# Optimization experiments

Measured on AMD Instinct MI355X. Metric: run time of the kernel, lower is better.

## Reference

```python
import jax, jax.numpy as jnp
import numpy as np

IN_FEATS, N_HIDDEN, NUM_LAYERS, N_CLASSES, CLS_HIDDEN = 166, 76, 2, 2, 510
T, N, E = 3, 100000, 1600000
RRELU_SLOPE = (1.0 / 8.0 + 1.0 / 3.0) / 2.0  # eval-mode RReLU = leaky relu with mean slope


def setup_inputs() -> dict:
    key = jax.random.key(0)
    ks = jax.random.split(key, 24)
    d = {}
    d['feats'] = jax.random.normal(ks[0], (T, N, IN_FEATS), jnp.float32)
    d['src'] = jax.random.randint(ks[1], (T, E), 0, N, jnp.int32)
    d['dst'] = jax.random.randint(ks[2], (T, E), 0, N, jnp.int32)
    # TopK scorers (uniform +-1/sqrt(feats))
    s0 = 1.0 / np.sqrt(IN_FEATS)
    s1 = 1.0 / np.sqrt(N_HIDDEN)
    d['scorer0'] = jax.random.uniform(ks[3], (IN_FEATS, 1), jnp.float32, -s0, s0)
    d['scorer1'] = jax.random.uniform(ks[4], (N_HIDDEN, 1), jnp.float32, -s1, s1)
    # GCN weights (xavier-ish)
    d['gcn_w0'] = jax.random.normal(ks[5], (IN_FEATS, N_HIDDEN), jnp.float32) * np.sqrt(2.0 / (IN_FEATS + N_HIDDEN))
    d['gcn_w1'] = jax.random.normal(ks[6], (N_HIDDEN, N_HIDDEN), jnp.float32) * np.sqrt(2.0 / (2 * N_HIDDEN))
    # GRU params, torch layout: W_ih [3H, H_in], W_hh [3H, H], gate order (r, z, n)
    g = 1.0 / np.sqrt(N_HIDDEN)
    H3 = 3 * N_HIDDEN
    d['gru0_wih'] = jax.random.uniform(ks[7], (H3, N_HIDDEN), jnp.float32, -g, g)
    d['gru0_whh'] = jax.random.uniform(ks[8], (H3, N_HIDDEN), jnp.float32, -g, g)
    d['gru0_bih'] = jax.random.uniform(ks[9], (H3,), jnp.float32, -g, g)
    d['gru0_bhh'] = jax.random.uniform(ks[10], (H3,), jnp.float32, -g, g)
    d['gru1_wih'] = jax.random.uniform(ks[11], (H3, N_HIDDEN), jnp.float32, -g, g)
    d['gru1_whh'] = jax.random.uniform(ks[12], (H3, N_HIDDEN), jnp.float32, -g, g)
    d['gru1_bih'] = jax.random.uniform(ks[13], (H3,), jnp.float32, -g, g)
    d['gru1_bhh'] = jax.random.uniform(ks[14], (H3,), jnp.float32, -g, g)
    # MLP
    m1 = 1.0 / np.sqrt(N_HIDDEN)
    m2 = 1.0 / np.sqrt(CLS_HIDDEN)
    d['mlp_w1'] = jax.random.uniform(ks[15], (N_HIDDEN, CLS_HIDDEN), jnp.float32, -m1, m1)
    d['mlp_b1'] = jax.random.uniform(ks[16], (CLS_HIDDEN,), jnp.float32, -m1, m1)
    d['mlp_w2'] = jax.random.uniform(ks[17], (CLS_HIDDEN, N_CLASSES), jnp.float32, -m2, m2)
    d['mlp_b2'] = jax.random.uniform(ks[18], (N_CLASSES,), jnp.float32, -m2, m2)
    return d


def _topk_pool(x, scorer, k):
    # x: [N, F]; returns X_tilde: [F, k]
    scores = (x @ scorer).ravel() / jnp.linalg.norm(scorer)
    vals, idx = jax.lax.top_k(scores, k)
    out = x[idx] * jnp.tanh(vals)[:, None]  # [k, F]
    return out.T


def _gru_step(x, h, wih, whh, bih, bhh):
    # x: [B, H_in], h: [B, H]; torch GRU gate order r, z, n
    gx = x @ wih.T + bih
    gh = h @ whh.T + bhh
    H = h.shape[1]
    rx, zx, nx = gx[:, :H], gx[:, H:2 * H], gx[:, 2 * H:]
    rh, zh, nh = gh[:, :H], gh[:, H:2 * H], gh[:, 2 * H:]
    r = jax.nn.sigmoid(rx + rh)
    z = jax.nn.sigmoid(zx + zh)
    n = jnp.tanh(nx + r * nh)
    return (1.0 - z) * n + z * h


def _graph_conv(x, W, src, dst, n_nodes):
    # DGL GraphConv, norm='both', bias=False, RReLU (eval) activation
    deg_out = jnp.zeros((n_nodes,), x.dtype).at[src].add(1.0)
    deg_in = jnp.zeros((n_nodes,), x.dtype).at[dst].add(1.0)
    norm_src = jnp.clip(deg_out, 1.0, None) ** -0.5
    norm_dst = jnp.clip(deg_in, 1.0, None) ** -0.5
    h = (x * norm_src[:, None]) @ W  # project first (small out dim)
    agg = jax.ops.segment_sum(h[src], dst, num_segments=n_nodes)
    out = agg * norm_dst[:, None]
    return jnp.where(out >= 0, out, out * RRELU_SLOPE)


def reference(feats, src, dst, scorer0, scorer1, gcn_w0, gcn_w1,
              gru0_wih, gru0_whh, gru0_bih, gru0_bhh,
              gru1_wih, gru1_whh, gru1_bih, gru1_bhh,
              mlp_w1, mlp_b1, mlp_w2, mlp_b2):
    scorers = [scorer0, scorer1]
    gcn_ws = [gcn_w0, gcn_w1]
    grus = [(gru0_wih, gru0_whh, gru0_bih, gru0_bhh),
            (gru1_wih, gru1_whh, gru1_bih, gru1_bhh)]
    feat_list = [feats[t] for t in range(T)]
    for i in range(NUM_LAYERS):
        W = gcn_ws[i]
        wih, whh, bih, bhh = grus[i]
        for t in range(T):
            x_tilde = _topk_pool(feat_list[t], scorers[i], N_HIDDEN)  # [F, k]
            W = _gru_step(x_tilde, W, wih, whh, bih, bhh)  # evolve weights
            feat_list[t] = _graph_conv(feat_list[t], W, src[t], dst[t], N)
    h = feat_list[-1]
    h = jax.nn.relu(h @ mlp_w1 + mlp_b1)
    return h @ mlp_w2 + mlp_b2
```

## Files before the change

### kernel.cpp

```cpp
#include <hip/hip_runtime.h>
#include <math.h>

#define NN 100000
#define EE 1600000
#define F0 166
#define HID 76
#define H3 228
#define CHID 510
#define SLOPE 0.22916666666666666f
#define CAND_MAX 4096
#define NBIN 4096
#define HPAD 20

#define BSH 9
#define BSZ 512
#define NBKT 196
#define CH 4096
#define NCHK 391
#define NBAND 13
#define AGG_NWG 7422

__device__ __forceinline__ unsigned f2key(float f){
    unsigned u = __float_as_uint(f);
    return (u & 0x80000000u) ? ~u : (u | 0x80000000u);
}
__device__ __forceinline__ float key2f(unsigned k){
    unsigned u = (k & 0x80000000u) ? (k & 0x7fffffffu) : ~k;
    return __uint_as_float(u);
}

__global__ void scorer_norms_k(const float* __restrict__ s0, const float* __restrict__ s1,
                               float* __restrict__ outn){
    __shared__ float red[256];
    int tid = threadIdx.x;
    float a = 0.f;
    for (int k = tid; k < F0; k += 256) a += s0[k]*s0[k];
    red[tid] = a; __syncthreads();
    for (int s = 128; s > 0; s >>= 1){ if (tid < s) red[tid] += red[tid+s]; __syncthreads(); }
    if (tid == 0) outn[0] = 1.0f/sqrtf(red[0]);
    __syncthreads();
    float b = 0.f;
    for (int k = tid; k < HID; k += 256) b += s1[k]*s1[k];
    red[tid] = b; __syncthreads();
    for (int s = 128; s > 0; s >>= 1){ if (tid < s) red[tid] += red[tid+s]; __syncthreads(); }
    if (tid == 0) outn[1] = 1.0f/sqrtf(red[0]);
}

__global__ void pad_k(const float* __restrict__ w1, const float* __restrict__ b1,
                      const float* __restrict__ w2, float* __restrict__ w1t,
                      float* __restrict__ b1p, float* __restrict__ w2p){
    int idx = blockIdx.x*256 + threadIdx.x;
    if (idx < 512*HID){
        int j = idx / HID, k = idx - j*HID;
        w1t[idx] = (j < CHID) ? w1[k*CHID + j] : 0.f;
    }
    if (idx < 512)  b1p[idx] = (idx < CHID)   ? b1[idx] : 0.f;
    if (idx < 1024) w2p[idx] = (idx < CHID*2) ? w2[idx] : 0.f;
}


__global__ __launch_bounds__(256) void p1_hist_k(const int* __restrict__ src, const int* __restrict__ dst,
                                                 int* __restrict__ bhS, int* __restrict__ bhD){
    __shared__ int hS[NBKT], hD[NBKT];
    int t = blockIdx.y, blk = blockIdx.x, tid = threadIdx.x;
    for (int i = tid; i < NBKT; i += 256){ hS[i] = 0; hD[i] = 0; }
    __syncthreads();
    size_t ebase = (size_t)t*EE + (size_t)blk*CH;
    int m = EE - blk*CH; if (m > CH) m = CH;
    for (int j = tid; j < m; j += 256){
        atomicAdd(&hS[src[ebase + j] >> BSH], 1);
        atomicAdd(&hD[dst[ebase + j] >> BSH], 1);
    }
    __syncthreads();
    for (int i = tid; i < NBKT; i += 256){
        bhS[((size_t)t*NBKT + i)*NCHK + blk] = hS[i];
        bhD[((size_t)t*NBKT + i)*NCHK + blk] = hD[i];
    }
}

__global__ __launch_bounds__(512) void p2_scan_k(int* __restrict__ bhS, int* __restrict__ bhD,
                                                 int* __restrict__ ctS, int* __restrict__ ctD){
    __shared__ int sd[512];
    int b = blockIdx.x, t = blockIdx.y, tid = threadIdx.x;
    for (int a = 0; a < 2; a++){
        int* bh = a ? bhD : bhS;
        int* ct = a ? ctD : ctS;
        int* row = bh + ((size_t)t*NBKT + b)*NCHK;
        int v = (tid < NCHK) ? row[tid] : 0;
        sd[tid] = v; __syncthreads();
        for (int off = 1; off < 512; off <<= 1){
            int x = (tid >= off) ? sd[tid - off] : 0;
            __syncthreads();
            sd[tid] += x;
            __syncthreads();
        }
        if (tid < NCHK) row[tid] = sd[tid] - v;
        if (tid == 511) ct[t*NBKT + b] = sd[511];
        __syncthreads();
    }
}

__global__ __launch_bounds__(256) void p3_base_k(const int* __restrict__ ctS, const int* __restrict__ ctD,
                                                 int* __restrict__ bbS, int* __restrict__ bbD){
    __shared__ int sd[256];
    int tid = threadIdx.x;
    for (int a = 0; a < 2; a++){
        const int* ct = a ? ctD : ctS;
        int* bb = a ? bbD : bbS;
        for (int t = 0; t < 3; t++){
            int v = (tid < NBKT) ? ct[t*NBKT + tid] : 0;
            sd[tid] = v; __syncthreads();
            for (int off = 1; off < 256; off <<= 1){
                int x = (tid >= off) ? sd[tid - off] : 0;
                __syncthreads();
                sd[tid] += x;
                __syncthreads();
            }
            if (tid < NBKT) bb[t*(NBKT+1) + tid] = sd[tid] - v;
            if (tid == 0)   bb[t*(NBKT+1) + NBKT] = EE;
            __syncthreads();
        }
    }
}

__global__ __launch_bounds__(256) void p4_scatter_k(const int* __restrict__ src, const int* __restrict__ dst,
                                                    const int* __restrict__ bhS, const int* __restrict__ bhD,
                                                    const int* __restrict__ bbS, const int* __restrict__ bbD,
                                                    int* __restrict__ srcpart,
                                                    unsigned long long* __restrict__ pairpart){
    __shared__ int baseS[NBKT], baseD[NBKT], cS[NBKT], cD[NBKT];
    int t = blockIdx.y, blk = blockIdx.x, tid = threadIdx.x;
    for (int i = tid; i < NBKT; i += 256){
        baseS[i] = bbS[t*(NBKT+1) + i] + bhS[((size_t)t*NBKT + i)*NCHK + blk];
        baseD[i] = bbD[t*(NBKT+1) + i] + bhD[((size_t)t*NBKT + i)*NCHK + blk];
        cS[i] = 0; cD[i] = 0;
    }
    __syncthreads();
    size_t ebase = (size_t)t*EE + (size_t)blk*CH;
    int m = EE - blk*CH; if (m > CH) m = CH;
    int* sp = srcpart + (size_t)t*EE;
    unsigned long long* pp = pairpart + (size_t)t*EE;
    for (int j = tid; j < m; j += 256){
        int s = src[ebase + j], d = dst[ebase + j];
        int bs = s >> BSH, bd = d >> BSH;
        int r0 = atomicAdd(&cS[bs], 1);
        sp[baseS[bs] + r0] = s;
        int r1 = atomicAdd(&cD[bd], 1);
        pp[baseD[bd] + r1] = ((unsigned long long)(unsigned)s << 32) | (unsigned)d;
    }
}

__global__ __launch_bounds__(256) void p5_degO_k(const int* __restrict__ srcpart,
                                                 const int* __restrict__ bbS,
                                                 float* __restrict__ nO){
    __shared__ int cnt[BSZ];
    int b = blockIdx.x, t = blockIdx.y, tid = threadIdx.x;
    for (int i = tid; i < BSZ; i += 256) cnt[i] = 0;
    __syncthreads();
    int st = bbS[t*(NBKT+1) + b], en = bbS[t*(NBKT+1) + b + 1];
    const int* sp = srcpart + (size_t)t*EE;
    for (int j = st + tid; j < en; j += 256) atomicAdd(&cnt[sp[j] & (BSZ-1)], 1);
    __syncthreads();
    int nb = b << BSH;
    for (int i = tid; i < BSZ; i += 256){
        int n = nb + i;
        if (n < NN){
            int o = cnt[i]; if (o < 1) o = 1;
            nO[t*NN + n] = 1.0f/sqrtf((float)o);
        }
    }
}

__global__ __launch_bounds__(512) void p6_csr_k(const unsigned long long* __restrict__ pairpart,
                                                const int* __restrict__ bbD,
                                                int* __restrict__ degI, int* __restrict__ rs,
                                                float* __restrict__ nI,
                                                int* __restrict__ col){
    __shared__ int cnt2[BSZ*NBAND];
    __shared__ int fc2[BSZ*NBAND];
    __shared__ int sd[BSZ];
    int b = blockIdx.x, t = blockIdx.y, tid = threadIdx.x;
    for (int i = tid; i < BSZ*NBAND; i += 512){ cnt2[i] = 0; fc2[i] = 0; }
    __syncthreads();
    int st = bbD[t*(NBKT+1) + b], en = bbD[t*(NBKT+1) + b + 1];
    const unsigned long long* pp = pairpart + (size_t)t*EE;
    for (int j = st + tid; j < en; j += 512){
        unsigned long long p = pp[j];
        int li   = (int)(p & (unsigned long long)(BSZ-1));
        int band = (int)(p >> 32) >> 13;
        atomicAdd(&cnt2[li*NBAND + band], 1);
    }
    __syncthreads();
    int rowcnt = 0;
    #pragma unroll
    for (int bb = 0; bb < NBAND; bb++) rowcnt += cnt2[tid*NBAND + bb];
    sd[tid] = rowcnt; __syncthreads();
    for (int off = 1; off < 512; off <<= 1){
        int x = (tid >= off) ? sd[tid - off] : 0;
        __syncthreads();
        sd[tid] += x;
        __syncthreads();
    }
    int rowEx = sd[tid] - rowcnt;
    int run = rowEx;
    #pragma unroll
    for (int bb = 0; bb < NBAND; bb++){
        int cvv = cnt2[tid*NBAND + bb];
        cnt2[tid*NBAND + bb] = run;
        run += cvv;
    }
    int nb = b << BSH;
    int n = nb + tid;
    if (n < NN){
        degI[t*NN + n] = rowcnt;
        rs[t*NN + n] = st + rowEx;
        int ii = rowcnt; if (ii < 1) ii = 1;
        nI[t*NN + n] = 1.0f/sqrtf((float)ii);
    }
    __syncthreads();
    int* ct = col + (size_t)t*EE;
    for (int j = st + tid; j < en; j += 512){
        unsigned long long p = pp[j];
        int s  = (int)(p >> 32);
        int li = (int)(p & (unsigned long long)(BSZ-1));
        int band = s >> 13;
        int r = atomicAdd(&fc2[li*NBAND + band], 1);
        ct[st + cnt2[li*NBAND + band] + r] = s;
    }
}


template<int F, int PAD>
__global__ __launch_bounds__(256) void score_k(const float* __restrict__ x,
                                               const float* __restrict__ scorer,
                                               const float* __restrict__ invn,
                                               float* __restrict__ scores,
                                               unsigned* hist){
    __shared__ float xs[64*PAD];
    __shared__ float part[256];
    int tid = threadIdx.x;
    int n0 = blockIdx.x*64;
    int nodes = NN - n0; if (nodes > 64) nodes = 64;
    for (int idx = tid; idx < nodes*F; idx += 256){
        int n = idx / F, k = idx - n*F;
        xs[n*PAD + k] = x[(size_t)(n0+n)*F + k];
    }
    __syncthreads();
    int w = __builtin_amdgcn_readfirstlane(tid >> 6);
    int lane = tid & 63;
    int k0 = (F*w) >> 2, k1 = (F*(w+1)) >> 2;
    const float* xrow = xs + lane*PAD;
    float s = 0.f;
    for (int k = k0; k < k1; k++) s += xrow[k]*scorer[k];
    part[w*64 + lane] = s;
    __syncthreads();
    if (tid < 64 && n0 + tid < NN){
        float tot = (part[tid] + part[64+tid] + part[128+tid] + part[192+tid]) * invn[0];
        scores[n0 + tid] = tot;
        atomicAdd(&hist[f2key(tot) >> 20], 1u);
    }
}

__global__ __launch_bounds__(256) void compact_k(const float* __restrict__ scores,
                                                 const unsigned* __restrict__ hist,
                                                 float* __restrict__ cv, int* __restrict__ ci, int* cnt){
    __shared__ unsigned cs[256];
    __shared__ int thr_s;
    int tid = threadIdx.x;
    unsigned s = 0;
    int base = NBIN - 1 - tid*16;
    for (int j = 0; j < 16; j++) s += hist[base - j];
    cs[tid] = s; __syncthreads();
    if (tid == 0){
        unsigned acc = 0; int c = 0;
        for (; c < 256; c++){ if (acc + cs[c] >= 76u) break; acc += cs[c]; }
        int b = NBIN - 1 - c*16;
        int sel = 0;
        for (int j = 0; j < 16; j++){
            acc += hist[b - j];
            if (acc >= 76u){ sel = b - j; break; }
        }
        thr_s = sel;
    }
    __syncthreads();
    int thr = thr_s;
    int n = blockIdx.x*256 + tid;
    if (n >= NN) return;
    float sv = scores[n];
    if ((int)(f2key(sv) >> 20) >= thr){
        int p = atomicAdd(cnt, 1);
        if (p < CAND_MAX){ cv[p] = sv; ci[p] = n; }
    }
}

__global__ __launch_bounds__(256) void topk_k(const float* __restrict__ cv,
                                              const int* __restrict__ ci,
                                              const int* __restrict__ cnt,
                                              int* __restrict__ topidx,
                                              float* __restrict__ tanhv){
    __shared__ unsigned long long keys[CAND_MAX];
    int tid = threadIdx.x;
    int M = *cnt; if (M > CAND_MAX) M = CAND_MAX;
    for (int i = tid; i < M; i += 256)
        keys[i] = ((unsigned long long)f2key(cv[i]) << 32) | (unsigned)(~ci[i]);
    __syncthreads();
    for (int i = tid; i < M; i += 256){
        unsigned long long ki = keys[i];
        int r = 0;
        for (int j = 0; j < M; j++) r += (keys[j] > ki) ? 1 : 0;
        if (r < 76){
            topidx[r] = (int)(~(unsigned)(ki & 0xffffffffu));
            tanhv[r]  = tanhf(key2f((unsigned)(ki >> 32)));
        }
    }
}

template<int F>
__global__ void gru_k(const float* __restrict__ cur, const int* __restrict__ topidx,
                      const float* __restrict__ tanhv, float* __restrict__ W,
                      float* __restrict__ Wt,
                      const float* __restrict__ wih, const float* __restrict__ whh,
                      const float* __restrict__ bih, const float* __restrict__ bhh){
    __shared__ float xr[HID], hr[HID], gx[H3], gh[H3];
    int r = blockIdx.x, tid = threadIdx.x;
    if (tid < HID){
        xr[tid] = cur[(size_t)topidx[tid]*F + r] * tanhv[tid];
        hr[tid] = W[r*HID + tid];
    }
    __syncthreads();
    if (tid < H3){
        const float* wi = wih + tid*HID;
        const float* wh = whh + tid*HID;
        float sa = 0.f, sb = 0.f;
        for (int k = 0; k < HID; k++){ sa += xr[k]*wi[k]; sb += hr[k]*wh[k]; }
        gx[tid] = bih[tid] + sa;
        gh[tid] = bhh[tid] + sb;
    }
    __syncthreads();
    if (tid < HID){
        float rr = 1.f/(1.f + expf(-(gx[tid] + gh[tid])));
        float zz = 1.f/(1.f + expf(-(gx[HID+tid] + gh[HID+tid])));
        float nn = tanhf(gx[2*HID+tid] + rr*gh[2*HID+tid]);
        float nv = (1.f - zz)*nn + zz*hr[tid];
        W[r*HID + tid] = nv;
        int c = tid >> 2, i = tid & 3;
        Wt[(c*F + r)*4 + i] = nv;
    }
}

template<int F, int PAD, int NB>
__global__ __launch_bounds__(256) void gemm_k(const float* __restrict__ x,
                                              const float* __restrict__ Wt,
                                              const float* __restrict__ nO,
                                              float* __restrict__ h){
    __shared__ __align__(16) float xs[NB*PAD];
    int tid = threadIdx.x;
    int n0 = blockIdx.x*NB;
    int nodes = NN - n0; if (nodes > NB) nodes = NB;
    for (int idx = tid; idx < nodes*F; idx += 256){
        int n = idx / F, k = idx - n*F;
        xs[n*PAD + k] = x[(size_t)(n0+n)*F + k];
    }
    __syncthreads();
    int w = __builtin_amdgcn_readfirstlane(tid >> 6);
    int lane = tid & 63;
    int c0 = w*5;
    const float4* Wt4 = (const float4*)Wt;
    float4 accA[5], accB[5];
    #pragma unroll
    for (int c = 0; c < 5; c++){
        accA[c] = make_float4(0.f,0.f,0.f,0.f);
        accB[c] = make_float4(0.f,0.f,0.f,0.f);
    }
    const float* xA = xs + lane*PAD;
    const float* xB = xs + ((NB==128) ? (lane+64)*PAD : lane*PAD);
    for (int k = 0; k < F; k++){
        float xa = xA[k];
        float xb = 0.f;
        if constexpr (NB == 128) xb = xB[k];
        #pragma unroll
        for (int c = 0; c < 5; c++){
            float4 wv = Wt4[(c0 + c)*F + k];
            accA[c].x += xa*wv.x; accA[c].y += xa*wv.y;
            accA[c].z += xa*wv.z; accA[c].w += xa*wv.w;
            if constexpr (NB == 128){
                accB[c].x += xb*wv.x; accB[c].y += xb*wv.y;
                accB[c].z += xb*wv.z; accB[c].w += xb*wv.w;
            }
        }
    }
    int nc = (w == 3) ? 4 : 5;
    int nA = n0 + lane;
    if (nA < NN){
        float nm = nO[nA];
        float4* h4 = (float4*)h + (size_t)nA*HPAD + c0;
        for (int c = 0; c < nc; c++){
            float4 a = accA[c];
            h4[c] = make_float4(a.x*nm, a.y*nm, a.z*nm, a.w*nm);
        }
    }
    if constexpr (NB == 128){
        int nB = n0 + 64 + lane;
        if (nB < NN){
            float nm = nO[nB];
            float4* h4 = (float4*)h + (size_t)nB*HPAD + c0;
            for (int c = 0; c < nc; c++){
                float4 a = accB[c];
                h4[c] = make_float4(a.x*nm, a.y*nm, a.z*nm, a.w*nm);
            }
        }
    }
}

__global__ __launch_bounds__(256) void agg_k(const int* __restrict__ rs, const int* __restrict__ degI,
                      const int* __restrict__ col, const float* __restrict__ h,
                      const float* __restrict__ nI, float* __restrict__ ft){
    int b0 = blockIdx.x;
    int xcd = b0 & 7, i0 = b0 >> 3;
    const int q = AGG_NWG >> 3;
    const int r8 = AGG_NWG & 7;
    int bs = (xcd < r8) ? (xcd*(q+1) + i0) : (r8*(q+1) + (xcd - r8)*q + i0);
    int idx = bs*256 + threadIdx.x;
    if (idx >= NN*19) return;
    int n = idx/19, c = idx - n*19;
    int st = rs[n], cnt = degI[n];
    const float4* h4 = (const float4*)h;
    float ax=0.f, ay=0.f, az=0.f, aw=0.f;
    int e = 0;
    for (; e + 8 <= cnt; e += 8){
        int s0 = col[st + e];
        int s1 = col[st + e + 1];
        int s2 = col[st + e + 2];
        int s3 = col[st + e + 3];
        int s4 = col[st + e + 4];
        int s5 = col[st + e + 5];
        int s6 = col[st + e + 6];
        int s7 = col[st + e + 7];
        float4 v0 = h4[(size_t)s0*HPAD + c];
        float4 v1 = h4[(size_t)s1*HPAD + c];
        float4 v2 = h4[(size_t)s2*HPAD + c];
        float4 v3 = h4[(size_t)s3*HPAD + c];
        float4 v4 = h4[(size_t)s4*HPAD + c];
        float4 v5 = h4[(size_t)s5*HPAD + c];
        float4 v6 = h4[(size_t)s6*HPAD + c];
        float4 v7 = h4[(size_t)s7*HPAD + c];
        ax += ((v0.x + v1.x) + (v2.x + v3.x)) + ((v4.x + v5.x) + (v6.x + v7.x));
        ay += ((v0.y + v1.y) + (v2.y + v3.y)) + ((v4.y + v5.y) + (v6.y + v7.y));
        az += ((v0.z + v1.z) + (v2.z + v3.z)) + ((v4.z + v5.z) + (v6.z + v7.z));
        aw += ((v0.w + v1.w) + (v2.w + v3.w)) + ((v4.w + v5.w) + (v6.w + v7.w));
    }
    for (; e + 2 <= cnt; e += 2){
        int s0 = col[st + e];
        int s1 = col[st + e + 1];
        float4 v0 = h4[(size_t)s0*HPAD + c];
        float4 v1 = h4[(size_t)s1*HPAD + c];
        ax += v0.x + v1.x; ay += v0.y + v1.y;
        az += v0.z + v1.z; aw += v0.w + v1.w;
    }
    if (e < cnt){
        int s = col[st + e];
        float4 v = h4[(size_t)s*HPAD + c];
        ax += v.x; ay += v.y; az += v.z; aw += v.w;
    }
    float nm = nI[n];
    ax*=nm; ay*=nm; az*=nm; aw*=nm;
    ax = ax >= 0.f ? ax : ax*SLOPE;
    ay = ay >= 0.f ? ay : ay*SLOPE;
    az = az >= 0.f ? az : az*SLOPE;
    aw = aw >= 0.f ? aw : aw*SLOPE;
    ((float4*)ft)[(size_t)n*19 + c] = make_float4(ax,ay,az,aw);
}

__global__ __launch_bounds__(512) void mlp3_k(const float* __restrict__ ft,
                                              const float* __restrict__ w1t,
                                              const float* __restrict__ b1p,
                                              const float* __restrict__ w2p,
                                              const float* __restrict__ b2,
                                              float* __restrict__ out){
    __shared__ __align__(16) float xs[128*HID];
    __shared__ __align__(16) float ws[256*HID];
    __shared__ float b1s[512];
    __shared__ float w2s[1024];
    int tid = threadIdx.x;
    int n0 = blockIdx.x*128;
    {
        int lim = ((NN - n0 < 128) ? (NN - n0) : 128)*19;
        const float4* g4 = (const float4*)(ft + (size_t)n0*HID);
        float4* s4 = (float4*)xs;
        for (int i = tid; i < 128*19; i += 512)
            s4[i] = (i < lim) ? g4[i] : make_float4(0.f,0.f,0.f,0.f);
    }
    b1s[tid] = b1p[tid];
    for (int i = tid; i < 1024; i += 512) w2s[i] = w2p[i];
    int wid = tid >> 6, lane = tid & 63;
    int wr = wid >> 2, wc = wid & 3;
    int a = lane >> 3, b = lane & 7;
    float p0[8], p1[8];
    #pragma unroll
    for (int i = 0; i < 8; i++){ p0[i] = 0.f; p1[i] = 0.f; }
    const float4* xbase = (const float4*)(xs + (wr*64 + a)*HID);
    for (int jb = 0; jb < 2; jb++){
        __syncthreads();
        {
            const float4* g4 = (const float4*)(w1t + (size_t)jb*256*HID);
            float4* s4 = (float4*)ws;
            for (int i = tid; i < 256*19; i += 512) s4[i] = g4[i];
        }
        __syncthreads();
        float acc[8][8];
        #pragma unroll
        for (int i = 0; i < 8; i++)
            #pragma unroll
            for (int m = 0; m < 8; m++) acc[i][m] = 0.f;
        const float4* wbase = (const float4*)(ws + (wc*64 + b)*HID);
        for (int k4 = 0; k4 < 19; k4++){
            float4 xv[8], wv[8];
            #pragma unroll
            for (int i = 0; i < 8; i++) xv[i] = xbase[i*(8*19) + k4];
            #pragma unroll
            for (int m = 0; m < 8; m++) wv[m] = wbase[m*(8*19) + k4];
            #pragma unroll
            for (int i = 0; i < 8; i++)
                #pragma unroll
                for (int m = 0; m < 8; m++){
                    acc[i][m] += xv[i].x*wv[m].x + xv[i].y*wv[m].y
                               + xv[i].z*wv[m].z + xv[i].w*wv[m].w;
                }
        }
        #pragma unroll
        for (int m = 0; m < 8; m++){
            int j = jb*256 + wc*64 + b + 8*m;
            float bias = b1s[j];
            float u0 = w2s[2*j], u1 = w2s[2*j+1];
            #pragma unroll
            for (int i = 0; i < 8; i++){
                float s = acc[i][m] + bias;
                s = fmaxf(s, 0.f);
                p0[i] += s*u0;
                p1[i] += s*u1;
            }
        }
    }
    #pragma unroll
    for (int off = 1; off < 8; off <<= 1){
        #pragma unroll
        for (int i = 0; i < 8; i++){
            p0[i] += __shfl_xor(p0[i], off, 64);
            p1[i] += __shfl_xor(p1[i], off, 64);
        }
    }
    __syncthreads();
    float* red = xs;
    if (b == 0){
        #pragma unroll
        for (int i = 0; i < 8; i++){
            int nl = wr*64 + a + 8*i;
            red[(wc*128 + nl)*2 + 0] = p0[i];
            red[(wc*128 + nl)*2 + 1] = p1[i];
        }
    }
    __syncthreads();
    if (tid < 256){
        int nl = tid >> 1, comp = tid & 1;
        float v = red[(0*128 + nl)*2 + comp] + red[(1*128 + nl)*2 + comp]
                + red[(2*128 + nl)*2 + comp] + red[(3*128 + nl)*2 + comp] + b2[comp];
        int n = n0 + nl;
        if (n < NN) out[(size_t)n*2 + comp] = v;
    }
}

extern "C" void kernel_launch(void* const* d_in, const int* in_sizes, int n_in,
                              void* d_out, int out_size, void* d_ws, size_t ws_size,
                              hipStream_t stream)
{
    (void)in_sizes; (void)n_in; (void)out_size; (void)ws_size;
    const float* feats   = (const float*)d_in[0];
    const int*   src     = (const int*)d_in[1];
    const int*   dst     = (const int*)d_in[2];
    const float* scorer0 = (const float*)d_in[3];
    const float* scorer1 = (const float*)d_in[4];
    const float* gcnw[2] = {(const float*)d_in[5],  (const float*)d_in[6]};
    const float* wih[2]  = {(const float*)d_in[7],  (const float*)d_in[11]};
    const float* whh[2]  = {(const float*)d_in[8],  (const float*)d_in[12]};
    const float* bih[2]  = {(const float*)d_in[9],  (const float*)d_in[13]};
    const float* bhh[2]  = {(const float*)d_in[10], (const float*)d_in[14]};
    const float* w1 = (const float*)d_in[15];
    const float* b1 = (const float*)d_in[16];
    const float* w2 = (const float*)d_in[17];
    const float* b2 = (const float*)d_in[18];
    float* out = (float*)d_out;

    char* p = (char*)d_ws;
    auto alloc = [&](size_t bytes) -> void* {
        void* r = (void*)p;
        p += (bytes + 255) & ~(size_t)255;
        return r;
    };
    float* ft[3];
    for (int t = 0; t < 3; t++) ft[t] = (float*)alloc((size_t)NN*HID*4);
    float* hbuf    = (float*)alloc((size_t)NN*HPAD*16);
    int*   col_all = (int*)alloc((size_t)3*EE*4);
    float* nO_all  = (float*)alloc((size_t)3*NN*4);
    float* nI_all  = (float*)alloc((size_t)3*NN*4);
    int*   rs_all  = (int*)alloc((size_t)3*NN*4);
    int*   dI_all  = (int*)alloc((size_t)3*NN*4);
    int* srcpart = (int*)alloc((size_t)3*EE*4);
    unsigned long long* pairpart = (unsigned long long*)alloc((size_t)3*EE*8);
    int* bhS = (int*)alloc((size_t)3*NBKT*NCHK*4);
    int* bhD = (int*)alloc((size_t)3*NBKT*NCHK*4);
    int* ctS = (int*)alloc((size_t)3*NBKT*4);
    int* ctD = (int*)alloc((size_t)3*NBKT*4);
    int* bbS = (int*)alloc((size_t)3*(NBKT+1)*4);
    int* bbD = (int*)alloc((size_t)3*(NBKT+1)*4);

    float*    scores = (float*)alloc((size_t)NN*4);
    float*    cv     = (float*)alloc(CAND_MAX*4);
    int*      ci     = (int*)alloc(CAND_MAX*4);
    int*      topidx = (int*)alloc(128*4);
    float*    tanhv  = (float*)alloc(128*4);
    float*    Wbuf   = (float*)alloc((size_t)F0*HID*4 + 256);
    float*    Wt     = (float*)alloc((size_t)19*F0*16 + 4096);
    float*    invn   = (float*)alloc(256);
    float*    w1t    = (float*)alloc((size_t)512*HID*4);
    float*    b1p    = (float*)alloc(512*4);
    float*    w2p    = (float*)alloc(1024*4);

    char* zbase = p;
    unsigned* hist6 = (unsigned*)alloc((size_t)6*NBIN*4);
    int*      ccnt6 = (int*)alloc(6*256);
    size_t zsize = (size_t)(p - zbase);

    const int gN  = (NN + 255)/256;
    const int gB  = (NN + 63)/64;
    const int gB2 = (NN + 127)/128;
    const int gM  = (NN + 127)/128;
    const int gP  = (512*HID + 255)/256;

    hipMemsetAsync(zbase, 0, zsize, stream);
    scorer_norms_k<<<1,256,0,stream>>>(scorer0, scorer1, invn);
    pad_k<<<gP,256,0,stream>>>(w1, b1, w2, w1t, b1p, w2p);

    p1_hist_k<<<dim3(NCHK,3),256,0,stream>>>(src, dst, bhS, bhD);
    p2_scan_k<<<dim3(NBKT,3),512,0,stream>>>(bhS, bhD, ctS, ctD);
    p3_base_k<<<1,256,0,stream>>>(ctS, ctD, bbS, bbD);
    p4_scatter_k<<<dim3(NCHK,3),256,0,stream>>>(src, dst, bhS, bhD, bbS, bbD, srcpart, pairpart);
    p5_degO_k<<<dim3(NBKT,3),256,0,stream>>>(srcpart, bbS, nO_all);
    p6_csr_k<<<dim3(NBKT,3),512,0,stream>>>(pairpart, bbD, dI_all, rs_all, nI_all, col_all);

    for (int i = 0; i < 2; i++){
        hipMemcpyAsync(Wbuf, gcnw[i], (size_t)((i==0)?F0:HID)*HID*4, hipMemcpyDeviceToDevice, stream);
        for (int t = 0; t < 3; t++){
            int q = i*3 + t;
            unsigned* hist = hist6 + (size_t)q*NBIN;
            int* ccnt = ccnt6 + q*64;
            const float* cur = (i == 0) ? (feats + (size_t)t*NN*F0) : ft[t];
            if (i == 0) score_k<F0,167><<<gB,256,0,stream>>>(cur, scorer0, invn+0, scores, hist);
            else        score_k<HID,77><<<gB,256,0,stream>>>(cur, scorer1, invn+1, scores, hist);
            compact_k<<<gN,256,0,stream>>>(scores, hist, cv, ci, ccnt);
            topk_k<<<1,256,0,stream>>>(cv, ci, ccnt, topidx, tanhv);
            if (i == 0){
                gru_k<F0><<<F0,256,0,stream>>>(cur, topidx, tanhv, Wbuf, Wt, wih[i], whh[i], bih[i], bhh[i]);
                gemm_k<F0,167,64><<<gB,256,0,stream>>>(cur, Wt, nO_all + (size_t)t*NN, hbuf);
            } else {
                gru_k<HID><<<HID,256,0,stream>>>(cur, topidx, tanhv, Wbuf, Wt, wih[i], whh[i], bih[i], bhh[i]);
                gemm_k<HID,77,128><<<gB2,256,0,stream>>>(cur, Wt, nO_all + (size_t)t*NN, hbuf);
            }
            agg_k<<<AGG_NWG,256,0,stream>>>(rs_all + (size_t)t*NN, dI_all + (size_t)t*NN,
                                            col_all + (size_t)t*EE, hbuf, nI_all + (size_t)t*NN, ft[t]);
        }
    }

    mlp3_k<<<gM,512,0,stream>>>(ft[2], w1t, b1p, w2p, b2, out);
}
```

Before: 2.509 ms.

## Pack edge pairs into 32-bit words and stream MLP weights from global memory

```diff
diff --git a/kernel.cpp b/kernel.cpp
--- a/kernel.cpp
+++ b/kernel.cpp
@@ -127,7 +127,7 @@
                                                     const int* __restrict__ bhS, const int* __restrict__ bhD,
                                                     const int* __restrict__ bbS, const int* __restrict__ bbD,
                                                     int* __restrict__ srcpart,
-                                                    unsigned long long* __restrict__ pairpart){
+                                                    unsigned* __restrict__ pairpart){
     __shared__ int baseS[NBKT], baseD[NBKT], cS[NBKT], cD[NBKT];
     int t = blockIdx.y, blk = blockIdx.x, tid = threadIdx.x;
     for (int i = tid; i < NBKT; i += 256){
@@ -139,14 +139,14 @@
     size_t ebase = (size_t)t*EE + (size_t)blk*CH;
     int m = EE - blk*CH; if (m > CH) m = CH;
     int* sp = srcpart + (size_t)t*EE;
-    unsigned long long* pp = pairpart + (size_t)t*EE;
+    unsigned* pp = pairpart + (size_t)t*EE;
     for (int j = tid; j < m; j += 256){
         int s = src[ebase + j], d = dst[ebase + j];
         int bs = s >> BSH, bd = d >> BSH;
         int r0 = atomicAdd(&cS[bs], 1);
         sp[baseS[bs] + r0] = s;
         int r1 = atomicAdd(&cD[bd], 1);
-        pp[baseD[bd] + r1] = ((unsigned long long)(unsigned)s << 32) | (unsigned)d;
+        pp[baseD[bd] + r1] = ((unsigned)s << BSH) | (unsigned)(d & (BSZ-1));
     }
 }
 
@@ -171,7 +171,7 @@
     }
 }
 
-__global__ __launch_bounds__(512) void p6_csr_k(const unsigned long long* __restrict__ pairpart,
+__global__ __launch_bounds__(512) void p6_csr_k(const unsigned* __restrict__ pairpart,
                                                 const int* __restrict__ bbD,
                                                 int* __restrict__ degI, int* __restrict__ rs,
                                                 float* __restrict__ nI,
@@ -183,11 +183,11 @@
     for (int i = tid; i < BSZ*NBAND; i += 512){ cnt2[i] = 0; fc2[i] = 0; }
     __syncthreads();
     int st = bbD[t*(NBKT+1) + b], en = bbD[t*(NBKT+1) + b + 1];
-    const unsigned long long* pp = pairpart + (size_t)t*EE;
+    const unsigned* pp = pairpart + (size_t)t*EE;
     for (int j = st + tid; j < en; j += 512){
-        unsigned long long p = pp[j];
-        int li   = (int)(p & (unsigned long long)(BSZ-1));
-        int band = (int)(p >> 32) >> 13;
+        unsigned p = pp[j];
+        int li   = (int)(p & (BSZ-1));
+        int band = (int)(p >> (BSH + 13));
         atomicAdd(&cnt2[li*NBAND + band], 1);
     }
     __syncthreads();
@@ -220,9 +220,9 @@
     __syncthreads();
     int* ct = col + (size_t)t*EE;
     for (int j = st + tid; j < en; j += 512){
-        unsigned long long p = pp[j];
-        int s  = (int)(p >> 32);
-        int li = (int)(p & (unsigned long long)(BSZ-1));
+        unsigned p = pp[j];
+        int s  = (int)(p >> BSH);
+        int li = (int)(p & (BSZ-1));
         int band = s >> 13;
         int r = atomicAdd(&fc2[li*NBAND + band], 1);
         ct[st + cnt2[li*NBAND + band] + r] = s;
@@ -471,71 +471,63 @@
     ((float4*)ft)[(size_t)n*19 + c] = make_float4(ax,ay,az,aw);
 }
 
-__global__ __launch_bounds__(512) void mlp3_k(const float* __restrict__ ft,
+__global__ __launch_bounds__(256) void mlp4_k(const float* __restrict__ ft,
                                               const float* __restrict__ w1t,
                                               const float* __restrict__ b1p,
                                               const float* __restrict__ w2p,
                                               const float* __restrict__ b2,
                                               float* __restrict__ out){
-    __shared__ __align__(16) float xs[128*HID];
-    __shared__ __align__(16) float ws[256*HID];
-    __shared__ float b1s[512];
-    __shared__ float w2s[1024];
+    __shared__ __align__(16) float xs[64*HID];
+    __shared__ float red[4*64*2];
     int tid = threadIdx.x;
-    int n0 = blockIdx.x*128;
+    int n0 = blockIdx.x*64;
     {
-        int lim = ((NN - n0 < 128) ? (NN - n0) : 128)*19;
+        int rem = NN - n0; if (rem > 64) rem = 64;
+        int lim = rem*19;
         const float4* g4 = (const float4*)(ft + (size_t)n0*HID);
         float4* s4 = (float4*)xs;
-        for (int i = tid; i < 128*19; i += 512)
+        for (int i = tid; i < 64*19; i += 256)
             s4[i] = (i < lim) ? g4[i] : make_float4(0.f,0.f,0.f,0.f);
     }
-    b1s[tid] = b1p[tid];
-    for (int i = tid; i < 1024; i += 512) w2s[i] = w2p[i];
-    int wid = tid >> 6, lane = tid & 63;
-    int wr = wid >> 2, wc = wid & 3;
+    __syncthreads();
+    int wc = __builtin_amdgcn_readfirstlane(tid >> 6);
+    int lane = tid & 63;
     int a = lane >> 3, b = lane & 7;
+    const float4* xbase = (const float4*)(xs) + a*19;
+    const float4* w4 = (const float4*)w1t;
     float p0[8], p1[8];
     #pragma unroll
     for (int i = 0; i < 8; i++){ p0[i] = 0.f; p1[i] = 0.f; }
-    const float4* xbase = (const float4*)(xs + (wr*64 + a)*HID);
     for (int jb = 0; jb < 2; jb++){
-        __syncthreads();
-        {
-            const float4* g4 = (const float4*)(w1t + (size_t)jb*256*HID);
-            float4* s4 = (float4*)ws;
-            for (int i = tid; i < 256*19; i += 512) s4[i] = g4[i];
-        }
-        __syncthreads();
+        int jbase = jb*256 + wc*64 + b;
         float acc[8][8];
         #pragma unroll
         for (int i = 0; i < 8; i++)
             #pragma unroll
             for (int m = 0; m < 8; m++) acc[i][m] = 0.f;
-        const float4* wbase = (const float4*)(ws + (wc*64 + b)*HID);
+        const float4* wrow = w4 + jbase*19;
         for (int k4 = 0; k4 < 19; k4++){
-            float4 xv[8], wv[8];
+            float4 wv[8];
             #pragma unroll
-            for (int i = 0; i < 8; i++) xv[i] = xbase[i*(8*19) + k4];
+            for (int m = 0; m < 8; m++) wv[m] = wrow[m*(8*19) + k4];
             #pragma unroll
-            for (int m = 0; m < 8; m++) wv[m] = wbase[m*(8*19) + k4];
-            #pragma unroll
-            for (int i = 0; i < 8; i++)
+            for (int i = 0; i < 8; i++){
+                float4 xv = xbase[i*(8*19) + k4];
                 #pragma unroll
                 for (int m = 0; m < 8; m++){
-                    acc[i][m] += xv[i].x*wv[m].x + xv[i].y*wv[m].y
-                               + xv[i].z*wv[m].z + xv[i].w*wv[m].w;
+                    acc[i][m] += xv.x*wv[m].x + xv.y*wv[m].y
+                               + xv.z*wv[m].z + xv.w*wv[m].w;
                 }
+            }
         }
         #pragma unroll
         for (int m = 0; m < 8; m++){
-            int j = jb*256 + wc*64 + b + 8*m;
-            float bias = b1s[j];
-            float u0 = w2s[2*j], u1 = w2s[2*j+1];
+            int j = jbase + 8*m;
+            float bias = b1p[j];
+            float u0 = w2p[2*j], u1 = w2p[2*j+1];
             #pragma unroll
             for (int i = 0; i < 8; i++){
-                float s = acc[i][m] + bias;
-                s = fmaxf(s, 0.f);
+                float s = fmaxf(acc[i][m] + bias, 0.f);
                 p0[i] += s*u0;
                 p1[i] += s*u1;
             }
@@ -549,21 +541,19 @@
             p1[i] += __shfl_xor(p1[i], off, 64);
         }
     }
-    __syncthreads();
-    float* red = xs;
     if (b == 0){
         #pragma unroll
         for (int i = 0; i < 8; i++){
-            int nl = wr*64 + a + 8*i;
-            red[(wc*128 + nl)*2 + 0] = p0[i];
-            red[(wc*128 + nl)*2 + 1] = p1[i];
-        }
-    }
-    __syncthreads();
-    if (tid < 256){
+            int nl = a + 8*i;
+            red[(wc*64 + nl)*2 + 0] = p0[i];
+            red[(wc*64 + nl)*2 + 1] = p1[i];
+        }
+    }
+    __syncthreads();
+    if (tid < 128){
         int nl = tid >> 1, comp = tid & 1;
-        float v = red[(0*128 + nl)*2 + comp] + red[(1*128 + nl)*2 + comp]
-                + red[(2*128 + nl)*2 + comp] + red[(3*128 + nl)*2 + comp] + b2[comp];
+        float v = red[(0*64 + nl)*2 + comp] + red[(1*64 + nl)*2 + comp]
+                + red[(2*64 + nl)*2 + comp] + red[(3*64 + nl)*2 + comp] + b2[comp];
         int n = n0 + nl;
         if (n < NN) out[(size_t)n*2 + comp] = v;
     }
@@ -605,7 +595,7 @@
     int*   rs_all  = (int*)alloc((size_t)3*NN*4);
     int*   dI_all  = (int*)alloc((size_t)3*NN*4);
     int* srcpart = (int*)alloc((size_t)3*EE*4);
-    unsigned long long* pairpart = (unsigned long long*)alloc((size_t)3*EE*8);
+    unsigned* pairpart = (unsigned*)alloc((size_t)3*EE*4);
     int* bhS = (int*)alloc((size_t)3*NBKT*NCHK*4);
     int* bhD = (int*)alloc((size_t)3*NBKT*NCHK*4);
     int* ctS = (int*)alloc((size_t)3*NBKT*4);
@@ -633,7 +623,6 @@
     const int gN  = (NN + 255)/256;
     const int gB  = (NN + 63)/64;
     const int gB2 = (NN + 127)/128;
-    const int gM  = (NN + 127)/128;
     const int gP  = (512*HID + 255)/256;
 
     hipMemsetAsync(zbase, 0, zsize, stream);
@@ -670,5 +659,5 @@
         }
     }
 
-    mlp3_k<<<gM,512,0,stream>>>(ft[2], w1t, b1p, w2p, b2, out);
-}
+    mlp4_k<<<gB,256,0,stream>>>(ft[2], w1t, b1p, w2p, b2, out);
+}
```

Result: no change. 2.518 ms (+0.4%).

## Batch top-k scoring across timesteps and pack edge pairs into 32 bits

Applied to the files above, without the earlier changes.

```diff
diff --git a/kernel.cpp b/kernel.cpp
--- a/kernel.cpp
+++ b/kernel.cpp
@@ -127,7 +127,7 @@
                                                     const int* __restrict__ bhS, const int* __restrict__ bhD,
                                                     const int* __restrict__ bbS, const int* __restrict__ bbD,
                                                     int* __restrict__ srcpart,
-                                                    unsigned long long* __restrict__ pairpart){
+                                                    unsigned* __restrict__ pairpart){
     __shared__ int baseS[NBKT], baseD[NBKT], cS[NBKT], cD[NBKT];
     int t = blockIdx.y, blk = blockIdx.x, tid = threadIdx.x;
     for (int i = tid; i < NBKT; i += 256){
@@ -139,14 +139,14 @@
     size_t ebase = (size_t)t*EE + (size_t)blk*CH;
     int m = EE - blk*CH; if (m > CH) m = CH;
     int* sp = srcpart + (size_t)t*EE;
-    unsigned long long* pp = pairpart + (size_t)t*EE;
+    unsigned* pp = pairpart + (size_t)t*EE;
     for (int j = tid; j < m; j += 256){
         int s = src[ebase + j], d = dst[ebase + j];
         int bs = s >> BSH, bd = d >> BSH;
         int r0 = atomicAdd(&cS[bs], 1);
         sp[baseS[bs] + r0] = s;
         int r1 = atomicAdd(&cD[bd], 1);
-        pp[baseD[bd] + r1] = ((unsigned long long)(unsigned)s << 32) | (unsigned)d;
+        pp[baseD[bd] + r1] = ((unsigned)s << BSH) | (unsigned)(d & (BSZ-1));
     }
 }
 
@@ -171,7 +171,7 @@
     }
 }
 
-__global__ __launch_bounds__(512) void p6_csr_k(const unsigned long long* __restrict__ pairpart,
+__global__ __launch_bounds__(512) void p6_csr_k(const unsigned* __restrict__ pairpart,
                                                 const int* __restrict__ bbD,
                                                 int* __restrict__ degI, int* __restrict__ rs,
                                                 float* __restrict__ nI,
@@ -183,11 +183,11 @@
     for (int i = tid; i < BSZ*NBAND; i += 512){ cnt2[i] = 0; fc2[i] = 0; }
     __syncthreads();
     int st = bbD[t*(NBKT+1) + b], en = bbD[t*(NBKT+1) + b + 1];
-    const unsigned long long* pp = pairpart + (size_t)t*EE;
+    const unsigned* pp = pairpart + (size_t)t*EE;
     for (int j = st + tid; j < en; j += 512){
-        unsigned long long p = pp[j];
-        int li   = (int)(p & (unsigned long long)(BSZ-1));
-        int band = (int)(p >> 32) >> 13;
+        unsigned p = pp[j];
+        int li   = (int)(p & (BSZ-1));
+        int band = (int)(p >> (BSH + 13));
         atomicAdd(&cnt2[li*NBAND + band], 1);
     }
     __syncthreads();
@@ -220,9 +220,9 @@
     __syncthreads();
     int* ct = col + (size_t)t*EE;
     for (int j = st + tid; j < en; j += 512){
-        unsigned long long p = pp[j];
-        int s  = (int)(p >> 32);
-        int li = (int)(p & (unsigned long long)(BSZ-1));
+        unsigned p = pp[j];
+        int s  = (int)(p >> BSH);
+        int li = (int)(p & (BSZ-1));
         int band = s >> 13;
         int r = atomicAdd(&fc2[li*NBAND + band], 1);
         ct[st + cnt2[li*NBAND + band] + r] = s;
@@ -231,13 +231,17 @@
 
 
 template<int F, int PAD>
-__global__ __launch_bounds__(256) void score_k(const float* __restrict__ x,
+__global__ __launch_bounds__(256) void score_k(const float* __restrict__ xbase,
                                                const float* __restrict__ scorer,
                                                const float* __restrict__ invn,
-                                               float* __restrict__ scores,
-                                               unsigned* hist){
+                                               float* __restrict__ scores_all,
+                                               unsigned* __restrict__ hist_all){
     __shared__ float xs[64*PAD];
     __shared__ float part[256];
+    int t = blockIdx.y;
+    const float* x = xbase + (size_t)t*NN*F;
+    float* scores = scores_all + (size_t)t*NN;
+    unsigned* hist = hist_all + (size_t)t*NBIN;
     int tid = threadIdx.x;
     int n0 = blockIdx.x*64;
     int nodes = NN - n0; if (nodes > 64) nodes = 64;
@@ -261,11 +265,18 @@
     }
 }
 
-__global__ __launch_bounds__(256) void compact_k(const float* __restrict__ scores,
-                                                 const unsigned* __restrict__ hist,
-                                                 float* __restrict__ cv, int* __restrict__ ci, int* cnt){
+__global__ __launch_bounds__(256) void compact_k(const float* __restrict__ scores_all,
+                                                 const unsigned* __restrict__ hist_all,
+                                                 float* __restrict__ cv_all, int* __restrict__ ci_all,
+                                                 int* __restrict__ cnt_all){
     __shared__ unsigned cs[256];
     __shared__ int thr_s;
+    int t = blockIdx.y;
+    const float* scores = scores_all + (size_t)t*NN;
+    const unsigned* hist = hist_all + (size_t)t*NBIN;
+    float* cv = cv_all + (size_t)t*CAND_MAX;
+    int*   ci = ci_all + (size_t)t*CAND_MAX;
+    int*   cnt = cnt_all + t*64;
     int tid = threadIdx.x;
     unsigned s = 0;
     int base = NBIN - 1 - tid*16;
@@ -293,14 +304,19 @@
     }
 }
 
-__global__ __launch_bounds__(256) void topk_k(const float* __restrict__ cv,
-                                              const int* __restrict__ ci,
-                                              const int* __restrict__ cnt,
-                                              int* __restrict__ topidx,
-                                              float* __restrict__ tanhv){
+__global__ __launch_bounds__(256) void topk_k(const float* __restrict__ cv_all,
+                                              const int* __restrict__ ci_all,
+                                              const int* __restrict__ cnt_all,
+                                              int* __restrict__ topidx_all,
+                                              float* __restrict__ tanhv_all){
     __shared__ unsigned long long keys[CAND_MAX];
+    int t = blockIdx.x;
+    const float* cv = cv_all + (size_t)t*CAND_MAX;
+    const int*   ci = ci_all + (size_t)t*CAND_MAX;
+    int* topidx = topidx_all + t*128;
+    float* tanhv = tanhv_all + t*128;
     int tid = threadIdx.x;
-    int M = *cnt; if (M > CAND_MAX) M = CAND_MAX;
+    int M = cnt_all[t*64]; if (M > CAND_MAX) M = CAND_MAX;
     for (int i = tid; i < M; i += 256)
         keys[i] = ((unsigned long long)f2key(cv[i]) << 32) | (unsigned)(~ci[i]);
     __syncthreads();
@@ -596,8 +612,7 @@
         p += (bytes + 255) & ~(size_t)255;
         return r;
     };
-    float* ft[3];
-    for (int t = 0; t < 3; t++) ft[t] = (float*)alloc((size_t)NN*HID*4);
+    float* ft_all = (float*)alloc((size_t)3*NN*HID*4);
     float* hbuf    = (float*)alloc((size_t)NN*HPAD*16);
     int*   col_all = (int*)alloc((size_t)3*EE*4);
     float* nO_all  = (float*)alloc((size_t)3*NN*4);
@@ -605,7 +620,7 @@
     int*   rs_all  = (int*)alloc((size_t)3*NN*4);
     int*   dI_all  = (int*)alloc((size_t)3*NN*4);
     int* srcpart = (int*)alloc((size_t)3*EE*4);
-    unsigned long long* pairpart = (unsigned long long*)alloc((size_t)3*EE*8);
+    unsigned* pairpart = (unsigned*)alloc((size_t)3*EE*4);
     int* bhS = (int*)alloc((size_t)3*NBKT*NCHK*4);
     int* bhD = (int*)alloc((size_t)3*NBKT*NCHK*4);
     int* ctS = (int*)alloc((size_t)3*NBKT*4);
@@ -613,17 +628,17 @@
     int* bbS = (int*)alloc((size_t)3*(NBKT+1)*4);
     int* bbD = (int*)alloc((size_t)3*(NBKT+1)*4);
 
-    float*    scores = (float*)alloc((size_t)NN*4);
-    float*    cv     = (float*)alloc(CAND_MAX*4);
-    int*      ci     = (int*)alloc(CAND_MAX*4);
-    int*      topidx = (int*)alloc(128*4);
-    float*    tanhv  = (float*)alloc(128*4);
-    float*    Wbuf   = (float*)alloc((size_t)F0*HID*4 + 256);
-    float*    Wt     = (float*)alloc((size_t)19*F0*16 + 4096);
-    float*    invn   = (float*)alloc(256);
-    float*    w1t    = (float*)alloc((size_t)512*HID*4);
-    float*    b1p    = (float*)alloc(512*4);
-    float*    w2p    = (float*)alloc(1024*4);
+    float*    scores3 = (float*)alloc((size_t)3*NN*4);
+    float*    cv3     = (float*)alloc((size_t)3*CAND_MAX*4);
+    int*      ci3     = (int*)alloc((size_t)3*CAND_MAX*4);
+    int*      topidx3 = (int*)alloc(3*128*4);
+    float*    tanhv3  = (float*)alloc(3*128*4);
+    float*    Wbuf    = (float*)alloc((size_t)F0*HID*4 + 256);
+    float*    Wt      = (float*)alloc((size_t)19*F0*16 + 4096);
+    float*    invn    = (float*)alloc(256);
+    float*    w1t     = (float*)alloc((size_t)512*HID*4);
+    float*    b1p     = (float*)alloc(512*4);
+    float*    w2p     = (float*)alloc(1024*4);
 
     char* zbase = p;
     unsigned* hist6 = (unsigned*)alloc((size_t)6*NBIN*4);
@@ -649,26 +664,28 @@
 
     for (int i = 0; i < 2; i++){
         hipMemcpyAsync(Wbuf, gcnw[i], (size_t)((i==0)?F0:HID)*HID*4, hipMemcpyDeviceToDevice, stream);
+        unsigned* hist3 = hist6 + (size_t)i*3*NBIN;
+        int*      cnt3  = ccnt6 + i*3*64;
+        if (i == 0) score_k<F0,167><<<dim3(gB,3),256,0,stream>>>(feats, scorer0, invn+0, scores3, hist3);
+        else        score_k<HID,77><<<dim3(gB,3),256,0,stream>>>(ft_all, scorer1, invn+1, scores3, hist3);
+        compact_k<<<dim3(gN,3),256,0,stream>>>(scores3, hist3, cv3, ci3, cnt3);
+        topk_k<<<3,256,0,stream>>>(cv3, ci3, cnt3, topidx3, tanhv3);
         for (int t = 0; t < 3; t++){
-            int q = i*3 + t;
-            unsigned* hist = hist6 + (size_t)q*NBIN;
-            int* ccnt = ccnt6 + q*64;
-            const float* cur = (i == 0) ? (feats + (size_t)t*NN*F0) : ft[t];
-            if (i == 0) score_k<F0,167><<<gB,256,0,stream>>>(cur, scorer0, invn+0, scores, hist);
-            else        score_k<HID,77><<<gB,256,0,stream>>>(cur, scorer1, invn+1, scores, hist);
-            compact_k<<<gN,256,0,stream>>>(scores, hist, cv, ci, ccnt);
-            topk_k<<<1,256,0,stream>>>(cv, ci, ccnt, topidx, tanhv);
+            const float* cur = (i == 0) ? (feats + (size_t)t*NN*F0) : (ft_all + (size_t)t*NN*HID);
             if (i == 0){
-                gru_k<F0><<<F0,256,0,stream>>>(cur, topidx, tanhv, Wbuf, Wt, wih[i], whh[i], bih[i], bhh[i]);
+                gru_k<F0><<<F0,256,0,stream>>>(cur, topidx3 + t*128, tanhv3 + t*128,
+                                               Wbuf, Wt, wih[i], whh[i], bih[i], bhh[i]);
                 gemm_k<F0,167,64><<<gB,256,0,stream>>>(cur, Wt, nO_all + (size_t)t*NN, hbuf);
             } else {
-                gru_k<HID><<<HID,256,0,stream>>>(cur, topidx, tanhv, Wbuf, Wt, wih[i], whh[i], bih[i], bhh[i]);
+                gru_k<HID><<<HID,256,0,stream>>>(cur, topidx3 + t*128, tanhv3 + t*128,
+                                                 Wbuf, Wt, wih[i], whh[i], bih[i], bhh[i]);
                 gemm_k<HID,77,128><<<gB2,256,0,stream>>>(cur, Wt, nO_all + (size_t)t*NN, hbuf);
             }
             agg_k<<<AGG_NWG,256,0,stream>>>(rs_all + (size_t)t*NN, dI_all + (size_t)t*NN,
-                                            col_all + (size_t)t*EE, hbuf, nI_all + (size_t)t*NN, ft[t]);
-        }
-    }
-
-    mlp3_k<<<gM,512,0,stream>>>(ft[2], w1t, b1p, w2p, b2, out);
-}
+                                            col_all + (size_t)t*EE, hbuf, nI_all + (size_t)t*NN,
+                                            ft_all + (size_t)t*NN*HID);
+        }
+    }
+
+    mlp3_k<<<gM,512,0,stream>>>(ft_all + (size_t)2*NN*HID, w1t, b1p, w2p, b2, out);
+}
```

Result: faster. 2.242 ms (-10.6%).
